# Optimization experiments

Measured on AMD Instinct MI355X. Metric: run time of the kernel, lower is better.

The kernel has to match this reference:

```python
import jax, jax.numpy as jnp
import numpy as np

N = 100000          # nodes
E = 1600000         # edges (avg degree 16)
DIN = 64
DOUT = 64
EXPERTS = 3
GATE_C = 4
TEMP = 101.0        # batch=0 < decay_lim: 100 - 0 + final_temperature(1.0)


def setup_inputs() -> dict:
    key = jax.random.key(0)
    ks = jax.random.split(key, 6)
    x = jax.random.normal(ks[0], (N, DIN), dtype=jnp.float32)
    edge_index = jax.random.randint(ks[1], (2, E), 0, N, dtype=jnp.int32)
    gate_features = jax.random.normal(ks[2], (N, GATE_C), dtype=jnp.float32)
    # per-expert GCN linear weights/bias (PyG GCNConv: lin then bias)
    W = jax.random.normal(ks[3], (EXPERTS, DIN, DOUT), dtype=jnp.float32) / np.sqrt(DIN).astype(np.float32)
    b = jnp.zeros((EXPERTS, DOUT), dtype=jnp.float32)
    # gating nn.Linear(gate_channels, experts, bias=False); stored as [GATE_C, EXPERTS] so y = gf @ Wg
    Wg = jax.random.normal(ks[4], (GATE_C, EXPERTS), dtype=jnp.float32) / np.sqrt(GATE_C).astype(np.float32)
    return {"x": x, "edge_index": edge_index, "gate_features": gate_features,
            "W": W, "b": b, "Wg": Wg}


def reference(x, edge_index, gate_features, W, b, Wg):
    n = x.shape[0]
    # --- GCN normalization with self-loops (PyG GCNConv defaults) ---
    loops = jnp.arange(n, dtype=edge_index.dtype)
    rows = jnp.concatenate([edge_index[0], loops])   # source nodes, [E+N]
    cols = jnp.concatenate([edge_index[1], loops])   # target nodes, [E+N]
    deg = jax.ops.segment_sum(jnp.ones(rows.shape, dtype=x.dtype), cols, num_segments=n)
    dinv = jnp.where(deg > 0, jax.lax.rsqrt(deg), 0.0)
    norm = dinv[rows] * dinv[cols]                   # [E+N]

    # --- gating network (softmax with decayed temperature) ---
    gate = jax.nn.softmax((gate_features @ Wg) / jnp.asarray(TEMP, x.dtype), axis=-1)  # [N, EXPERTS]

    # --- experts: GCN conv -> ReLU -> gate-weighted accumulation ---
    out = jnp.zeros((n, W.shape[-1]), dtype=x.dtype)
    for i in range(W.shape[0]):                      # small fixed expert count
        xw = x @ W[i]                                # [N, DOUT]
        msg = xw[rows] * norm[:, None]               # gather + scale, [E+N, DOUT]
        agg = jax.ops.segment_sum(msg, cols, num_segments=n) + b[i]
        out = out + gate[:, i:i + 1] * jax.nn.relu(agg)
    return out
```

## Files before the change

### kernel.cpp

```cpp
#include <hip/hip_runtime.h>
#include <hip/hip_bf16.h>

#define NN 100000
#define NE 1600000
#define NT 6250

#define NBUCK  511
#define BRANGE 196
#define CAPB   3584
#define CHUNK  2048
#define NCH    782

typedef __attribute__((ext_vector_type(8))) short bf16x8;
typedef __attribute__((ext_vector_type(4))) float f32x4;

__device__ inline float2 bf16x2_unpack(unsigned v) {
    float2 r;
    r.x = __uint_as_float(v << 16);
    r.y = __uint_as_float(v & 0xffff0000u);
    return r;
}
__device__ inline unsigned bf16x2_pack(float a, float b) {
    __hip_bfloat162 h2(__float2bfloat16(a), __float2bfloat16(b));
    unsigned u;
    __builtin_memcpy(&u, &h2, 4);
    return u;
}

__global__ __launch_bounds__(256) void bin_kernel(const int* __restrict__ rows,
                                                  const int* __restrict__ cols,
                                                  int* __restrict__ cur,
                                                  unsigned* __restrict__ eb) {
    __shared__ int hist[512];
    __shared__ int excl[512];
    __shared__ int lcur[512];
    __shared__ int gbase[512];
    __shared__ int s2[256];
    __shared__ unsigned staged[CHUNK];
    __shared__ unsigned short bktarr[CHUNK];
    int t = threadIdx.x;
    int base = blockIdx.x * CHUNK;
    int cnt = min(CHUNK, NE - base);

    hist[t] = 0; hist[t + 256] = 0;
    __syncthreads();
    #pragma unroll
    for (int k = 0; k < CHUNK / 256; k++) {
        int i = k * 256 + t;
        if (i < cnt) {
            int c = cols[base + i];
            atomicAdd(&hist[(unsigned)c / BRANGE], 1);
        }
    }
    __syncthreads();
    int a0 = hist[2 * t], a1 = hist[2 * t + 1];
    s2[t] = a0 + a1;
    __syncthreads();
    #pragma unroll
    for (int off = 1; off < 256; off <<= 1) {
        int v = (t >= off) ? s2[t - off] : 0;
        __syncthreads();
        s2[t] += v;
        __syncthreads();
    }
    int pe = (t > 0) ? s2[t - 1] : 0;
    excl[2 * t] = pe;      excl[2 * t + 1] = pe + a0;
    lcur[2 * t] = pe;      lcur[2 * t + 1] = pe + a0;
    gbase[2 * t]     = a0 ? atomicAdd(cur + 2 * t * 16, a0) : 0;
    gbase[2 * t + 1] = a1 ? atomicAdd(cur + (2 * t + 1) * 16, a1) : 0;
    __syncthreads();
    #pragma unroll
    for (int k = 0; k < CHUNK / 256; k++) {
        int i = k * 256 + t;
        if (i < cnt) {
            int c = cols[base + i];
            int r = rows[base + i];
            int bkt = (unsigned)c / BRANGE;
            int lp = atomicAdd(&lcur[bkt], 1);
            staged[lp] = ((unsigned)(c - bkt * BRANGE) << 24) | (unsigned)r;
            bktarr[lp] = (unsigned short)bkt;
        }
    }
    __syncthreads();
    #pragma unroll
    for (int k = 0; k < CHUNK / 256; k++) {
        int i = k * 256 + t;
        if (i < cnt) {
            int bkt = bktarr[i];
            int pos = gbase[bkt] + (i - excl[bkt]);
            if (pos < CAPB) eb[(size_t)bkt * CAPB + pos] = staged[i];
        }
    }
}

__global__ __launch_bounds__(512) void sortn_kernel(const int* __restrict__ cur,
                                                    const unsigned* __restrict__ eb,
                                                    int* __restrict__ srcs2,
                                                    int2* __restrict__ nsd) {
    __shared__ unsigned recs[CAPB];
    __shared__ unsigned srcl[CAPB];
    __shared__ int hist[256];
    __shared__ int lcur[256];
    int b = blockIdx.x, t = threadIdx.x;
    if (t < 256) hist[t] = 0;
    __syncthreads();
    int cnt = min(cur[b * 16], CAPB);
    const unsigned* seg = eb + (size_t)b * CAPB;
    for (int i = t; i < cnt; i += 512) {
        unsigned r = seg[i];
        recs[i] = r;
        atomicAdd(&hist[r >> 24], 1);
    }
    __syncthreads();
    if (t < 64) {
        int e = t * 4;
        int h0 = hist[e], h1 = hist[e + 1], h2 = hist[e + 2], h3 = hist[e + 3];
        int lsum = h0 + h1 + h2 + h3;
        int inc = lsum;
        #pragma unroll
        for (int off = 1; off < 64; off <<= 1) {
            int v = __shfl_up(inc, off);
            if (t >= off) inc += v;
        }
        int ex = inc - lsum;
        int e0 = ex, e1 = ex + h0, e2 = e1 + h1, e3 = e2 + h2;
        lcur[e] = e0; lcur[e + 1] = e1; lcur[e + 2] = e2; lcur[e + 3] = e3;
        int n = b * BRANGE + e;
        if (e     < BRANGE && n     < NN) nsd[n]     = make_int2(e0, h0);
        if (e + 1 < BRANGE && n + 1 < NN) nsd[n + 1] = make_int2(e1, h1);
        if (e + 2 < BRANGE && n + 2 < NN) nsd[n + 2] = make_int2(e2, h2);
        if (e + 3 < BRANGE && n + 3 < NN) nsd[n + 3] = make_int2(e3, h3);
    }
    __syncthreads();
    for (int i = t; i < cnt; i += 512) {
        unsigned r = recs[i];
        int p = atomicAdd(&lcur[r >> 24], 1);
        srcl[p] = r & 0xFFFFFFu;
    }
    __syncthreads();
    for (int i = t; i < cnt; i += 512)
        srcs2[(size_t)b * CAPB + i] = (int)srcl[i];
}

__global__ __launch_bounds__(256) void xscale_kernel(const float* __restrict__ x,
                                                     const int2* __restrict__ nsd,
                                                     unsigned* __restrict__ xs) {
    int i = blockIdx.x * 256 + threadIdx.x;
    int n = i >> 5;
    int d = (i & 31) * 2;
    float2 v = *(const float2*)(x + (size_t)n * 64 + d);
    float dv = rsqrtf((float)(nsd[n].y + 1));
    xs[i] = bf16x2_pack(v.x * dv, v.y * dv);
}

__global__ __launch_bounds__(256) void gather_kernel(const int* __restrict__ srcs2,
                                                     const int2* __restrict__ nsd,
                                                     const unsigned* __restrict__ xs,
                                                     unsigned* __restrict__ hbu) {
    int lane = threadIdx.x & 63;
    int wave = threadIdx.x >> 6;
    int g  = lane >> 4;
    int gl = lane & 15;
    int gb = g << 4;

    int n = blockIdx.x * 16 + wave * 4 + g;
    int2 sd = nsd[n];
    int deg = sd.y;
    int bkt = (unsigned)n / BRANGE;
    const int* seg = srcs2 + (size_t)bkt * CAPB + sd.x;
    const uint2* xsv = (const uint2*)xs;

    float4 acc = make_float4(0.f, 0.f, 0.f, 0.f);
    for (int base = 0; base < deg; base += 16) {
        int idx = 0;
        if (base + gl < deg) idx = seg[base + gl];
        int s0 = __shfl(idx, gb);
        uint2 v[16];
        #pragma unroll
        for (int j = 0; j < 16; j++) {
            int s = __shfl(idx, gb + j);
            s = (base + j < deg) ? s : s0;
            v[j] = xsv[(size_t)s * 16 + gl];
        }
        #pragma unroll
        for (int j = 0; j < 16; j++) {
            if (base + j < deg) {
                float2 f0 = bf16x2_unpack(v[j].x);
                float2 f1 = bf16x2_unpack(v[j].y);
                acc.x += f0.x; acc.y += f0.y;
                acc.z += f1.x; acc.w += f1.y;
            }
        }
    }
    uint2 svu = xsv[(size_t)n * 16 + gl];
    float2 sv0 = bf16x2_unpack(svu.x);
    float2 sv1 = bf16x2_unpack(svu.y);
    float dn = rsqrtf((float)(deg + 1));
    uint2 o;
    o.x = bf16x2_pack((acc.x + sv0.x) * dn, (acc.y + sv0.y) * dn);
    o.y = bf16x2_pack((acc.z + sv1.x) * dn, (acc.w + sv1.y) * dn);
    ((uint2*)hbu)[(size_t)n * 16 + gl] = o;
}

__global__ void wpack_kernel(const float* __restrict__ W, __hip_bfloat16* __restrict__ Bp) {
    int idx = blockIdx.x * 256 + threadIdx.x;
    if (idx >= 12288) return;
    int j    = idx & 7;
    int lane = (idx >> 3) & 63;
    int rest = idx >> 9;
    int t    = rest % 12;
    int kh   = rest / 12;
    int k    = kh * 32 + (lane >> 4) * 8 + j;
    int col  = t * 16 + (lane & 15);
    int i    = col >> 6;
    int d    = col & 63;
    Bp[idx] = __float2bfloat16(W[(i * 64 + k) * 64 + d]);
}

__global__ __launch_bounds__(256) void mfma_kernel(const __hip_bfloat16* __restrict__ hb,
                                                   const short* __restrict__ Bp,
                                                   const float* __restrict__ b,
                                                   const float* __restrict__ gf,
                                                   const float* __restrict__ Wg,
                                                   float* __restrict__ out) {
    int wave = threadIdx.x >> 6;
    int lane = threadIdx.x & 63;
    int tile = blockIdx.x * 4 + wave;
    if (tile >= NT) return;
    int n0 = tile * 16;
    int m = lane & 15, quad = lane >> 4;

    const short* hrow = (const short*)hb + ((size_t)(n0 + m)) * 64 + quad * 8;
    bf16x8 a0 = *(const bf16x8*)(hrow);
    bf16x8 a1 = *(const bf16x8*)(hrow + 32);

    f32x4 acc[12];
    #pragma unroll
    for (int t = 0; t < 12; t++) acc[t] = (f32x4)(0.0f);

    #pragma unroll
    for (int kh = 0; kh < 2; kh++) {
        bf16x8 a = kh ? a1 : a0;
        #pragma unroll
        for (int t = 0; t < 12; t++) {
            bf16x8 bf = *(const bf16x8*)(Bp + ((size_t)((kh * 12 + t) * 64 + lane)) * 8);
            acc[t] = __builtin_amdgcn_mfma_f32_16x16x32_bf16(a, bf, acc[t], 0, 0, 0);
        }
    }

    float wg[12];
    #pragma unroll
    for (int k = 0; k < 12; k++) wg[k] = Wg[k];

    #pragma unroll
    for (int reg = 0; reg < 4; reg++) {
        int n = n0 + quad * 4 + reg;
        float4 g = ((const float4*)gf)[n];
        float l0 = (g.x*wg[0] + g.y*wg[3] + g.z*wg[6] + g.w*wg[9])  * (1.0f/101.0f);
        float l1 = (g.x*wg[1] + g.y*wg[4] + g.z*wg[7] + g.w*wg[10]) * (1.0f/101.0f);
        float l2 = (g.x*wg[2] + g.y*wg[5] + g.z*wg[8] + g.w*wg[11]) * (1.0f/101.0f);
        float mx = fmaxf(l0, fmaxf(l1, l2));
        float e0 = __expf(l0 - mx), e1 = __expf(l1 - mx), e2 = __expf(l2 - mx);
        float inv = 1.0f / (e0 + e1 + e2);
        float g0 = e0 * inv, g1 = e1 * inv, g2 = e2 * inv;
        #pragma unroll
        for (int dpos = 0; dpos < 4; dpos++) {
            int d = dpos * 16 + m;
            float v0 = acc[0*4 + dpos][reg] + b[0*64 + d];
            float v1 = acc[1*4 + dpos][reg] + b[1*64 + d];
            float v2 = acc[2*4 + dpos][reg] + b[2*64 + d];
            float o = g0 * fmaxf(v0, 0.f) + g1 * fmaxf(v1, 0.f) + g2 * fmaxf(v2, 0.f);
            out[(size_t)n * 64 + d] = o;
        }
    }
}

extern "C" void kernel_launch(void* const* d_in, const int* in_sizes, int n_in,
                              void* d_out, int out_size, void* d_ws, size_t ws_size,
                              hipStream_t stream) {
    const float* x  = (const float*)d_in[0];
    const int*   ei = (const int*)d_in[1];
    const float* gf = (const float*)d_in[2];
    const float* W  = (const float*)d_in[3];
    const float* b  = (const float*)d_in[4];
    const float* Wg = (const float*)d_in[5];
    float* out = (float*)d_out;
    const int* rows = ei;
    const int* cols = ei + NE;

    char* ws = (char*)d_ws;
    size_t off = 0;
    auto alloc = [&](size_t bytes) {
        char* p = ws + off;
        off = (off + bytes + 255) & ~(size_t)255;
        return p;
    };
    int*            cur   = (int*)alloc(512 * 16 * 4);
    unsigned*       eb    = (unsigned*)alloc((size_t)NBUCK * CAPB * 4);
    int*            srcs2 = (int*)alloc((size_t)NBUCK * CAPB * 4);
    int2*           nsd   = (int2*)alloc((size_t)NN * 8);
    unsigned*       xs    = (unsigned*)alloc((size_t)NN * 32 * 4);
    unsigned*       hbu   = (unsigned*)alloc((size_t)NN * 32 * 4);
    __hip_bfloat16* Bp    = (__hip_bfloat16*)alloc(12288 * 2);

    hipMemsetAsync(cur, 0, 512 * 16 * 4, stream);

    bin_kernel<<<NCH, 256, 0, stream>>>(rows, cols, cur, eb);
    sortn_kernel<<<NBUCK, 512, 0, stream>>>(cur, eb, srcs2, nsd);
    xscale_kernel<<<NN * 32 / 256, 256, 0, stream>>>(x, nsd, xs);
    wpack_kernel<<<48, 256, 0, stream>>>(W, Bp);
    gather_kernel<<<NN / 16, 256, 0, stream>>>(srcs2, nsd, xs, hbu);
    mfma_kernel<<<(NT + 3) / 4, 256, 0, stream>>>((const __hip_bfloat16*)hbu,
                                                  (const short*)Bp, b, gf, Wg, out);
}
```

Measured before the change: 178.5 us.

## Fuse x scaling into sort kernel and use per-wave histograms in binning

The bin kernel now keeps per-wave privatized histograms and replaces the 256-step barrier scan with a single-wave shuffle scan, and it caches column indices in registers instead of reloading them. The sort kernel also uses per-wave histograms with per-wave base offsets, which removes the shared recs buffer, and it takes over the degree-normalised bf16 conversion of x for its own node range, so the separate xscale launch is gone. This is meant to cut LDS atomic contention, barrier count, redundant global loads and one kernel launch. In exchange it adds register pressure and extra LDS in the sort kernel, and the per-wave placement order inside a node's edge list changes.

```diff
diff --git a/kernel.cpp b/kernel.cpp
--- a/kernel.cpp
+++ b/kernel.cpp
@@ -31,49 +31,64 @@
                                                   const int* __restrict__ cols,
                                                   int* __restrict__ cur,
                                                   unsigned* __restrict__ eb) {
-    __shared__ int hist[512];
+    __shared__ int hist4[4][512];
     __shared__ int excl[512];
     __shared__ int lcur[512];
     __shared__ int gbase[512];
-    __shared__ int s2[256];
     __shared__ unsigned staged[CHUNK];
     __shared__ unsigned short bktarr[CHUNK];
     int t = threadIdx.x;
+    int wave = t >> 6;
     int base = blockIdx.x * CHUNK;
     int cnt = min(CHUNK, NE - base);
 
-    hist[t] = 0; hist[t + 256] = 0;
-    __syncthreads();
+    #pragma unroll
+    for (int u = t; u < 2048; u += 256) ((int*)hist4)[u] = 0;
+    __syncthreads();
+
+    int cbuf[CHUNK / 256];
     #pragma unroll
     for (int k = 0; k < CHUNK / 256; k++) {
         int i = k * 256 + t;
-        if (i < cnt) {
-            int c = cols[base + i];
-            atomicAdd(&hist[(unsigned)c / BRANGE], 1);
-        }
-    }
-    __syncthreads();
-    int a0 = hist[2 * t], a1 = hist[2 * t + 1];
-    s2[t] = a0 + a1;
-    __syncthreads();
-    #pragma unroll
-    for (int off = 1; off < 256; off <<= 1) {
-        int v = (t >= off) ? s2[t - off] : 0;
-        __syncthreads();
-        s2[t] += v;
-        __syncthreads();
-    }
-    int pe = (t > 0) ? s2[t - 1] : 0;
-    excl[2 * t] = pe;      excl[2 * t + 1] = pe + a0;
-    lcur[2 * t] = pe;      lcur[2 * t + 1] = pe + a0;
-    gbase[2 * t]     = a0 ? atomicAdd(cur + 2 * t * 16, a0) : 0;
-    gbase[2 * t + 1] = a1 ? atomicAdd(cur + (2 * t + 1) * 16, a1) : 0;
-    __syncthreads();
+        int c = (i < cnt) ? cols[base + i] : -1;
+        cbuf[k] = c;
+        if (c >= 0) atomicAdd(&hist4[wave][(unsigned)c / BRANGE], 1);
+    }
+    __syncthreads();
+
+    if (t < 64) {
+        int carry = 0;
+        #pragma unroll
+        for (int k = 0; k < 8; k++) {
+            int e = k * 64 + t;
+            int h = hist4[0][e] + hist4[1][e] + hist4[2][e] + hist4[3][e];
+            int inc = h;
+            #pragma unroll
+            for (int off = 1; off < 64; off <<= 1) {
+                int v = __shfl_up(inc, off);
+                if (t >= off) inc += v;
+            }
+            int ex = carry + inc - h;
+            excl[e] = ex;
+            lcur[e] = ex;
+            hist4[0][e] = h;
+            carry += __shfl(inc, 63);
+        }
+    }
+    __syncthreads();
+
+    #pragma unroll
+    for (int u = t; u < 512; u += 256) {
+        int h = hist4[0][u];
+        gbase[u] = h ? atomicAdd(cur + u * 16, h) : 0;
+    }
+    __syncthreads();
+
     #pragma unroll
     for (int k = 0; k < CHUNK / 256; k++) {
         int i = k * 256 + t;
-        if (i < cnt) {
-            int c = cols[base + i];
+        int c = cbuf[k];
+        if (c >= 0) {
             int r = rows[base + i];
             int bkt = (unsigned)c / BRANGE;
             int lp = atomicAdd(&lcur[bkt], 1);
@@ -82,6 +97,7 @@
         }
     }
     __syncthreads();
+
     #pragma unroll
     for (int k = 0; k < CHUNK / 256; k++) {
         int i = k * 256 + t;
@@ -95,62 +111,82 @@
 
 __global__ __launch_bounds__(512) void sortn_kernel(const int* __restrict__ cur,
                                                     const unsigned* __restrict__ eb,
+                                                    const float* __restrict__ x,
                                                     int* __restrict__ srcs2,
-                                                    int2* __restrict__ nsd) {
-    __shared__ unsigned recs[CAPB];
+                                                    int2* __restrict__ nsd,
+                                                    unsigned* __restrict__ xs) {
     __shared__ unsigned srcl[CAPB];
-    __shared__ int hist[256];
-    __shared__ int lcur[256];
+    __shared__ int whist[8][256];
+    __shared__ int wbase[8][256];
+    __shared__ int ndeg[256];
     int b = blockIdx.x, t = threadIdx.x;
-    if (t < 256) hist[t] = 0;
-    __syncthreads();
+    int wave = t >> 6;
+
+    #pragma unroll
+    for (int u = t; u < 2048; u += 512) ((int*)whist)[u] = 0;
+    __syncthreads();
+
     int cnt = min(cur[b * 16], CAPB);
     const unsigned* seg = eb + (size_t)b * CAPB;
-    for (int i = t; i < cnt; i += 512) {
-        unsigned r = seg[i];
-        recs[i] = r;
-        atomicAdd(&hist[r >> 24], 1);
-    }
-    __syncthreads();
+    unsigned rr[CAPB / 512];
+    #pragma unroll
+    for (int k = 0; k < CAPB / 512; k++) {
+        int i = k * 512 + t;
+        unsigned r = (i < cnt) ? seg[i] : 0xFFFFFFFFu;
+        rr[k] = r;
+        if (r != 0xFFFFFFFFu) atomicAdd(&whist[wave][r >> 24], 1);
+    }
+    __syncthreads();
+
     if (t < 64) {
-        int e = t * 4;
-        int h0 = hist[e], h1 = hist[e + 1], h2 = hist[e + 2], h3 = hist[e + 3];
-        int lsum = h0 + h1 + h2 + h3;
-        int inc = lsum;
-        #pragma unroll
-        for (int off = 1; off < 64; off <<= 1) {
-            int v = __shfl_up(inc, off);
-            if (t >= off) inc += v;
-        }
-        int ex = inc - lsum;
-        int e0 = ex, e1 = ex + h0, e2 = e1 + h1, e3 = e2 + h2;
-        lcur[e] = e0; lcur[e + 1] = e1; lcur[e + 2] = e2; lcur[e + 3] = e3;
-        int n = b * BRANGE + e;
-        if (e     < BRANGE && n     < NN) nsd[n]     = make_int2(e0, h0);
-        if (e + 1 < BRANGE && n + 1 < NN) nsd[n + 1] = make_int2(e1, h1);
-        if (e + 2 < BRANGE && n + 2 < NN) nsd[n + 2] = make_int2(e2, h2);
-        if (e + 3 < BRANGE && n + 3 < NN) nsd[n + 3] = make_int2(e3, h3);
-    }
-    __syncthreads();
-    for (int i = t; i < cnt; i += 512) {
-        unsigned r = recs[i];
-        int p = atomicAdd(&lcur[r >> 24], 1);
-        srcl[p] = r & 0xFFFFFFu;
-    }
-    __syncthreads();
+        int carry = 0;
+        #pragma unroll
+        for (int k = 0; k < 4; k++) {
+            int e = k * 64 + t;
+            int hw[8];
+            int h = 0;
+            #pragma unroll
+            for (int w = 0; w < 8; w++) { hw[w] = whist[w][e]; h += hw[w]; }
+            int inc = h;
+            #pragma unroll
+            for (int off = 1; off < 64; off <<= 1) {
+                int v = __shfl_up(inc, off);
+                if (t >= off) inc += v;
+            }
+            int ex = carry + inc - h;
+            int acc = ex;
+            #pragma unroll
+            for (int w = 0; w < 8; w++) { wbase[w][e] = acc; acc += hw[w]; }
+            ndeg[e] = h;
+            int n = b * BRANGE + e;
+            if (e < BRANGE && n < NN) nsd[n] = make_int2(ex, h);
+            carry += __shfl(inc, 63);
+        }
+    }
+    __syncthreads();
+
+    #pragma unroll
+    for (int k = 0; k < CAPB / 512; k++) {
+        unsigned r = rr[k];
+        if (r != 0xFFFFFFFFu) {
+            int p = atomicAdd(&wbase[wave][r >> 24], 1);
+            srcl[p] = r & 0xFFFFFFu;
+        }
+    }
+    __syncthreads();
+
     for (int i = t; i < cnt; i += 512)
         srcs2[(size_t)b * CAPB + i] = (int)srcl[i];
-}
-
-__global__ __launch_bounds__(256) void xscale_kernel(const float* __restrict__ x,
-                                                     const int2* __restrict__ nsd,
-                                                     unsigned* __restrict__ xs) {
-    int i = blockIdx.x * 256 + threadIdx.x;
-    int n = i >> 5;
-    int d = (i & 31) * 2;
-    float2 v = *(const float2*)(x + (size_t)n * 64 + d);
-    float dv = rsqrtf((float)(nsd[n].y + 1));
-    xs[i] = bf16x2_pack(v.x * dv, v.y * dv);
+
+    int nloc = min(BRANGE, NN - b * BRANGE);
+    for (int i = t; i < nloc * 32; i += 512) {
+        int nl = i >> 5;
+        int d = i & 31;
+        int n = b * BRANGE + nl;
+        float2 v = *(const float2*)(x + (size_t)n * 64 + d * 2);
+        float dv = rsqrtf((float)(ndeg[nl] + 1));
+        xs[(size_t)n * 32 + d] = bf16x2_pack(v.x * dv, v.y * dv);
+    }
 }
 
 __global__ __launch_bounds__(256) void gather_kernel(const int* __restrict__ srcs2,
@@ -306,8 +342,7 @@
     hipMemsetAsync(cur, 0, 512 * 16 * 4, stream);
 
     bin_kernel<<<NCH, 256, 0, stream>>>(rows, cols, cur, eb);
-    sortn_kernel<<<NBUCK, 512, 0, stream>>>(cur, eb, srcs2, nsd);
-    xscale_kernel<<<NN * 32 / 256, 256, 0, stream>>>(x, nsd, xs);
+    sortn_kernel<<<NBUCK, 512, 0, stream>>>(cur, eb, x, srcs2, nsd, xs);
     wpack_kernel<<<48, 256, 0, stream>>>(W, Bp);
     gather_kernel<<<NN / 16, 256, 0, stream>>>(srcs2, nsd, xs, hbu);
     mfma_kernel<<<(NT + 3) / 4, 256, 0, stream>>>((const __hip_bfloat16*)hbu,
```

Measured after the change: 190.9 us. 6.9% more time.
